# Kernel optimization log

Hardware: AMD Instinct MI355X
Metric: run time of the kernel (lower is better)

## Reference

```python
import jax, jax.numpy as jnp
import numpy as np

N, K = 262144, 8
IN_F, H_F, OUT_F = 16, 128, 16
NEG_SLOPE = 0.01  # torch LeakyReLU default


def setup_inputs() -> dict:
    key = jax.random.key(0)
    ks = jax.random.split(key, 10)
    h = jax.random.normal(ks[0], (N, IN_F), dtype=jnp.float32)
    pos = jax.random.uniform(ks[1], (N, 3), dtype=jnp.float32)
    nbr_idx = jax.random.randint(ks[2], (N, K), 0, N)

    def xavier(k, shape):
        fan_in, fan_out = shape[0], shape[1]
        a = jnp.sqrt(6.0 / (fan_in + fan_out))
        return jax.random.uniform(k, shape, jnp.float32, -a, a)

    W0 = xavier(ks[3], (K * IN_F, H_F))
    b0 = xavier(ks[4], (1, H_F))
    W1 = xavier(ks[5], (K * H_F, H_F))
    b1 = xavier(ks[6], (1, H_F))
    W2 = xavier(ks[7], (K * H_F, OUT_F))
    b2 = xavier(ks[8], (1, OUT_F))
    return {"h": h, "pos": pos, "nbr_idx": nbr_idx,
            "W0": W0, "b0": b0, "W1": W1, "b1": b1, "W2": W2, "b2": b2}


def _layer(h, pos, nbr_idx, W, b, activation):
    # gather neighbor messages and positions: [N, K, F], [N, K, 3]
    msgs = h[nbr_idx]
    src_pos = pos[nbr_idx]
    diff = pos[:, None, :] - src_pos                       # [N, K, 3]
    dist = jnp.sqrt(jnp.sum(diff * diff, axis=2, keepdims=True))  # [N, K, 1]
    dist = jnp.where(dist == 0, jnp.float32(0.5), dist)
    wow = (msgs / dist).reshape(h.shape[0], -1)            # [N, K*F]
    out = wow @ W + b
    if activation:
        out = jnp.where(out >= 0, out, NEG_SLOPE * out)
    return out


def reference(h, pos, nbr_idx, W0, b0, W1, b1, W2, b2):
    h1 = _layer(h, pos, nbr_idx, W0, b0, False)   # input layer
    h2 = _layer(h1, pos, nbr_idx, W1, b1, True)   # hidden layer (LeakyReLU)
    h3 = _layer(h2, pos, nbr_idx, W2, b2, False)  # output layer
    return h3
```

## Files before the change

### kernel.cpp

```cpp
#include <hip/hip_runtime.h>
#include <hip/hip_fp16.h>


typedef _Float16 f16x8 __attribute__((ext_vector_type(8)));
typedef float f32x4 __attribute__((ext_vector_type(4)));

#define NNODES 262144

__device__ __forceinline__ void gload_lds16(const __half* g, __half* l) {
    __builtin_amdgcn_global_load_lds(
        (const __attribute__((address_space(1))) unsigned int*)g,
        (__attribute__((address_space(3))) unsigned int*)l, 16, 0, 0);
}

__global__ __launch_bounds__(256) void conv_h_kernel(const float* __restrict__ h,
                                                     __half* __restrict__ h16, int n) {
    int i = blockIdx.x * 256 + threadIdx.x;
    if (i < n) h16[i] = __float2half(h[i]);
}

__global__ __launch_bounds__(256) void prep_edges_kernel(const float* __restrict__ pos,
                                                         const int* __restrict__ nbr,
                                                         __half* __restrict__ invd, int n_edges) {
    int e = blockIdx.x * 256 + threadIdx.x;
    if (e >= n_edges) return;
    int i = e >> 3;
    int n = nbr[e];
    float dx = pos[i * 3 + 0] - pos[n * 3 + 0];
    float dy = pos[i * 3 + 1] - pos[n * 3 + 1];
    float dz = pos[i * 3 + 2] - pos[n * 3 + 2];
    float d = sqrtf(dx * dx + dy * dy + dz * dz);
    if (d == 0.0f) d = 0.5f;
    invd[e] = __float2half((1.0f / d) * 0.00390625f);
}

__global__ __launch_bounds__(256) void shuffle_w_kernel(const float* __restrict__ W,
                                                        __half* __restrict__ Wf,
                                                        int KT, int FO) {
    int e = blockIdx.x * 256 + threadIdx.x;
    if (e >= KT * FO) return;
    int j = e & 7;
    int lane = (e >> 3) & 63;
    int rest = e >> 9;
    int NT = FO >> 4;
    int t = rest % NT;
    int s = rest / NT;
    int k = s * 32 + (lane >> 4) * 8 + j;
    int n = t * 16 + (lane & 15);
    Wf[e] = __float2half(W[k * FO + n]);
}

__global__ __launch_bounds__(256) void shuffle_w2s_kernel(const float* __restrict__ W2,
                                                          __half* __restrict__ Wf) {
    int e = blockIdx.x * 256 + threadIdx.x;
    if (e >= 128 * 128) return;
    int j = e & 7;
    int lane = (e >> 3) & 63;
    int rest = e >> 9;
    int t = rest % 8;
    int s = rest / 8;
    int k = s * 32 + (lane >> 4) * 8 + j;
    Wf[e] = __float2half(W2[(size_t)(t * 128 + k) * 16 + (lane & 15)]);
}

__global__ __launch_bounds__(256) void layer0_kernel(
    const __half* __restrict__ hprev, const __half* __restrict__ invd,
    const int* __restrict__ nbr, const __half* __restrict__ Wf,
    const float* __restrict__ bias, __half* __restrict__ outp) {
    __shared__ __align__(16) __half Bs[16384];

    const int tid = threadIdx.x;
    const int wave = tid >> 6;
    const int lane = tid & 63;
    const int quad = lane >> 4;
    const int lmod = lane & 15;
    const int mbase = blockIdx.x * 128 + wave * 16 + lmod;

    int idx[2][8];
    f16x8 invr[2];
#pragma unroll
    for (int mt = 0; mt < 2; ++mt) {
        const int m = mbase + mt * 64;
        const int4* nrow = (const int4*)(nbr + (size_t)m * 8);
        const int4 iA = nrow[0];
        const int4 iB = nrow[1];
        idx[mt][0] = iA.x; idx[mt][1] = iA.y; idx[mt][2] = iA.z; idx[mt][3] = iA.w;
        idx[mt][4] = iB.x; idx[mt][5] = iB.y; idx[mt][6] = iB.z; idx[mt][7] = iB.w;
        invr[mt] = *(const f16x8*)(invd + (size_t)m * 8);
    }

    f32x4 acc[2][8];
#pragma unroll
    for (int mt = 0; mt < 2; ++mt)
#pragma unroll
        for (int t = 0; t < 8; ++t) acc[mt][t] = f32x4{0.f, 0.f, 0.f, 0.f};

    {
        const uint4* src = (const uint4*)Wf;
        uint4* dst = (uint4*)Bs;
#pragma unroll
        for (int i = 0; i < 8; ++i) dst[i * 256 + tid] = src[i * 256 + tid];
    }
    __syncthreads();

#pragma unroll
    for (int s = 0; s < 4; ++s) {
        const int nb = 2 * s + (quad >> 1);
        f16x8 as[2];
#pragma unroll
        for (int mt = 0; mt < 2; ++mt) {
            f16x8 av = *(const f16x8*)(hprev + (size_t)idx[mt][nb] * 16 + (quad & 1) * 8);
            as[mt] = av * invr[mt][nb];
        }
#pragma unroll
        for (int t = 0; t < 8; ++t) {
            f16x8 b = *(const f16x8*)(Bs + ((size_t)(s * 8 + t) * 64 + lane) * 8);
#pragma unroll
            for (int mt = 0; mt < 2; ++mt)
                acc[mt][t] = __builtin_amdgcn_mfma_f32_16x16x32_f16(as[mt], b, acc[mt][t], 0, 0, 0);
        }
    }

#pragma unroll
    for (int mt = 0; mt < 2; ++mt) {
        const int rbase = blockIdx.x * 128 + mt * 64 + wave * 16 + quad * 4;
#pragma unroll
        for (int t = 0; t < 8; ++t) {
            const int col = t * 16 + lmod;
            const float bv = bias[col];
#pragma unroll
            for (int rr = 0; rr < 4; ++rr) {
                float v = acc[mt][t][rr] * 256.0f + bv;
                outp[(size_t)(rbase + rr) * 128 + col] = __float2half(v);
            }
        }
    }
}

__device__ __forceinline__ int off16(int seg, int row) {
    return seg * 64 + (row & ~15) + ((row ^ seg) & 15);
}

__global__ __launch_bounds__(256, 4) void layer1p_kernel(
    const __half* __restrict__ hprev, const __half* __restrict__ invd,
    const int* __restrict__ nbr, const __half* __restrict__ Wf,
    const __half* __restrict__ Wf2s, const float* __restrict__ bias,
    __half* __restrict__ Pout) {
    __shared__ __align__(16) __half As[2][8192];

    const int tid = threadIdx.x;
    const int wave = tid >> 6;
    const int lane = tid & 63;
    const int quad = lane >> 4;
    const int lmod = lane & 15;
    const int rowblk = blockIdx.x * 64;

    int grow2[4];
#pragma unroll
    for (int i = 0; i < 4; ++i) {
        const int row = (lane & 48) | ((lane & 15) ^ (wave * 4 + i));
        grow2[i] = rowblk + row;
    }

    int idxA[4], idxB[4], idxR[2][4];
#pragma unroll
    for (int i = 0; i < 4; ++i) {
        const int* nb_ = nbr + (size_t)grow2[i] * 8;
        idxA[i] = nb_[0];
        idxB[i] = nb_[1];
        idxR[0][i] = nb_[2];
    }

    f16x8 invF[4];
#pragma unroll
    for (int m = 0; m < 4; ++m)
        invF[m] = *(const f16x8*)(invd + (size_t)(rowblk + m * 16 + lmod) * 8);

    int roff4[4];
#pragma unroll
    for (int ks = 0; ks < 4; ++ks) {
        const int seg = ks * 4 + quad;
        roff4[ks] = (seg * 64 + ((lmod ^ seg) & 15)) * 8;
    }

    const __half* WfB = Wf + ((size_t)(wave * 2) * 64 + lane) * 8;

    f16x8 Bc[2][2], Bn[2][2];
#pragma unroll
    for (int ks2 = 0; ks2 < 2; ++ks2)
#pragma unroll
        for (int tl = 0; tl < 2; ++tl)
            Bc[ks2][tl] = *(const f16x8*)(WfB + (size_t)(ks2 * 8 + tl) * 512);

#pragma unroll
    for (int i = 0; i < 4; ++i)
        gload_lds16(hprev + (size_t)idxA[i] * 128 + (wave * 4 + i) * 8,
                    &As[0][(size_t)(wave * 256 + i * 64) * 8]);

    f32x4 acc[4][2];
#pragma unroll
    for (int m = 0; m < 4; ++m) { acc[m][0] = f32x4{0.f,0.f,0.f,0.f}; acc[m][1] = f32x4{0.f,0.f,0.f,0.f}; }

    __syncthreads();

#pragma unroll
    for (int nb = 0; nb < 8; ++nb) {
        const int cur = nb & 1;
        if (nb < 7) {
#pragma unroll
            for (int i = 0; i < 4; ++i) {
                const int id = (nb == 0) ? idxB[i] : idxR[(nb + 1) & 1][i];
                gload_lds16(hprev + (size_t)id * 128 + (wave * 4 + i) * 8,
                            &As[cur ^ 1][(size_t)(wave * 256 + i * 64) * 8]);
            }
        }
        if (nb < 5) {
#pragma unroll
            for (int i = 0; i < 4; ++i)
                idxR[(nb + 1) & 1][i] = nbr[(size_t)grow2[i] * 8 + nb + 3];
        }
#pragma unroll
        for (int h = 0; h < 2; ++h) {
            const int p = nb * 2 + h;
            if (p < 15) {
#pragma unroll
                for (int ks2 = 0; ks2 < 2; ++ks2)
#pragma unroll
                    for (int tl = 0; tl < 2; ++tl)
                        Bn[ks2][tl] = *(const f16x8*)(WfB + (size_t)(((p + 1) * 2 + ks2) * 8 + tl) * 512);
            }
#pragma unroll
            for (int m = 0; m < 4; ++m) {
#pragma unroll
                for (int ks2 = 0; ks2 < 2; ++ks2) {
                    const int ks = h * 2 + ks2;
                    f16x8 a = *(const f16x8*)(&As[cur][roff4[ks] + m * 128]);
                    a = a * invF[m][nb];
                    acc[m][0] = __builtin_amdgcn_mfma_f32_16x16x32_f16(a, Bc[ks2][0], acc[m][0], 0, 0, 0);
                    acc[m][1] = __builtin_amdgcn_mfma_f32_16x16x32_f16(a, Bc[ks2][1], acc[m][1], 0, 0, 0);
                }
            }
#pragma unroll
            for (int ks2 = 0; ks2 < 2; ++ks2) {
                Bc[ks2][0] = Bn[ks2][0];
                Bc[ks2][1] = Bn[ks2][1];
            }
        }
        if (nb < 7) __syncthreads();
    }

    __half* As0 = &As[0][0];
#pragma unroll
    for (int m = 0; m < 4; ++m) {
#pragma unroll
        for (int tl = 0; tl < 2; ++tl) {
            const int col = wave * 32 + tl * 16 + lmod;
            const float bv = bias[col];
            const int sg = col >> 3;
            const int jj = col & 7;
#pragma unroll
            for (int rr = 0; rr < 4; ++rr) {
                const int row = m * 16 + quad * 4 + rr;
                float v = acc[m][tl][rr] * 256.0f + bv;
                v = (v >= 0.f) ? v : 0.01f * v;
                As0[off16(sg, row) * 8 + jj] = __float2half(v);
            }
        }
    }
    __syncthreads();

    const __half* WfB2 = Wf2s + ((size_t)(wave * 2) * 64 + lane) * 8;
    f16x8 B2[4][2];
#pragma unroll
    for (int ks = 0; ks < 4; ++ks)
#pragma unroll
        for (int tl = 0; tl < 2; ++tl)
            B2[ks][tl] = *(const f16x8*)(WfB2 + (size_t)(ks * 8 + tl) * 512);

    f32x4 acc2[4][2];
#pragma unroll
    for (int m = 0; m < 4; ++m) { acc2[m][0] = f32x4{0.f,0.f,0.f,0.f}; acc2[m][1] = f32x4{0.f,0.f,0.f,0.f}; }
#pragma unroll
    for (int m = 0; m < 4; ++m) {
#pragma unroll
        for (int ks = 0; ks < 4; ++ks) {
            f16x8 a2 = *(const f16x8*)(&As0[roff4[ks] + m * 128]);
            acc2[m][0] = __builtin_amdgcn_mfma_f32_16x16x32_f16(a2, B2[ks][0], acc2[m][0], 0, 0, 0);
            acc2[m][1] = __builtin_amdgcn_mfma_f32_16x16x32_f16(a2, B2[ks][1], acc2[m][1], 0, 0, 0);
        }
    }

#pragma unroll
    for (int m = 0; m < 4; ++m) {
#pragma unroll
        for (int tl = 0; tl < 2; ++tl) {
            const int col = wave * 32 + tl * 16 + lmod;
#pragma unroll
            for (int rr = 0; rr < 4; ++rr) {
                const int grow = rowblk + m * 16 + quad * 4 + rr;
                Pout[(size_t)grow * 128 + col] = __float2half(acc2[m][tl][rr]);
            }
        }
    }
}

__global__ __launch_bounds__(256) void reduce_kernel(
    const __half* __restrict__ P, const __half* __restrict__ invd,
    const int* __restrict__ nbr, const float* __restrict__ b2,
    float* __restrict__ outp) {
    const int d = blockIdx.x * 256 + threadIdx.x;

    const int4* nrow = (const int4*)(nbr + (size_t)d * 8);
    const int4 iA = nrow[0];
    const int4 iB = nrow[1];
    const int idx[8] = {iA.x, iA.y, iA.z, iA.w, iB.x, iB.y, iB.z, iB.w};
    const f16x8 iv = *(const f16x8*)(invd + (size_t)d * 8);

    f16x8 lo[8], hi[8];
#pragma unroll
    for (int k = 0; k < 8; ++k) {
        const __half* p = P + (size_t)idx[k] * 128 + k * 16;
        lo[k] = *(const f16x8*)p;
        hi[k] = *(const f16x8*)(p + 8);
    }

    float acc[16];
#pragma unroll
    for (int c = 0; c < 16; ++c) acc[c] = 0.f;
#pragma unroll
    for (int k = 0; k < 8; ++k) {
        const float w = (float)iv[k];
#pragma unroll
        for (int c = 0; c < 8; ++c) {
            acc[c] += w * (float)lo[k][c];
            acc[c + 8] += w * (float)hi[k][c];
        }
    }

    float4 o[4];
#pragma unroll
    for (int q = 0; q < 4; ++q) {
        o[q].x = acc[q * 4 + 0] * 256.0f + b2[q * 4 + 0];
        o[q].y = acc[q * 4 + 1] * 256.0f + b2[q * 4 + 1];
        o[q].z = acc[q * 4 + 2] * 256.0f + b2[q * 4 + 2];
        o[q].w = acc[q * 4 + 3] * 256.0f + b2[q * 4 + 3];
    }
    float4* dst = (float4*)(outp + (size_t)d * 16);
#pragma unroll
    for (int q = 0; q < 4; ++q) dst[q] = o[q];
}

extern "C" void kernel_launch(void* const* d_in, const int* in_sizes, int n_in,
                              void* d_out, int out_size, void* d_ws, size_t ws_size,
                              hipStream_t stream) {
    const float* h   = (const float*)d_in[0];
    const float* pos = (const float*)d_in[1];
    const int*   nbr = (const int*)d_in[2];
    const float* W0  = (const float*)d_in[3];
    const float* b0  = (const float*)d_in[4];
    const float* W1  = (const float*)d_in[5];
    const float* b1  = (const float*)d_in[6];
    const float* W2  = (const float*)d_in[7];
    const float* b2  = (const float*)d_in[8];

    const int N = NNODES;

    char* w = (char*)d_ws;
    __half* h1 = (__half*)w;
    __half* P  = (__half*)(w + (size_t)67108864);
    __half* invd2 = (__half*)w;

    char* ob = (char*)d_out;
    __half* invd = (__half*)(ob + 0);
    __half* h16  = (__half*)(ob + 4194304);
    __half* W0f  = (__half*)(ob + 12582912);
    __half* W1f  = (__half*)(ob + 12615680);
    __half* Wf2s = (__half*)(ob + 12877824);

    conv_h_kernel<<<(N * 16 + 255) / 256, 256, 0, stream>>>(h, h16, N * 16);
    prep_edges_kernel<<<(N * 8 + 255) / 256, 256, 0, stream>>>(pos, nbr, invd, N * 8);
    shuffle_w_kernel<<<(128 * 128 + 255) / 256, 256, 0, stream>>>(W0, W0f, 128, 128);
    shuffle_w_kernel<<<(1024 * 128 + 255) / 256, 256, 0, stream>>>(W1, W1f, 1024, 128);
    shuffle_w2s_kernel<<<(128 * 128 + 255) / 256, 256, 0, stream>>>(W2, Wf2s);

    layer0_kernel<<<N / 128, 256, 0, stream>>>(h16, invd, nbr, W0f, b0, h1);
    layer1p_kernel<<<N / 64, 256, 0, stream>>>(h1, invd, nbr, W1f, Wf2s, b1, P);

    (void)hipMemcpyAsync(invd2, invd, 4194304, hipMemcpyDeviceToDevice, stream);

    reduce_kernel<<<N / 256, 256, 0, stream>>>(P, invd2, nbr, b2, (float*)d_out);
}
```

Before: 355.2 us.

## Replace direct global-to-LDS gathers with register-staged gathers pre-scaled by inverse distance

```diff
diff --git a/kernel.cpp b/kernel.cpp
--- a/kernel.cpp
+++ b/kernel.cpp
@@ -6,12 +6,6 @@
 typedef float f32x4 __attribute__((ext_vector_type(4)));
 
 #define NNODES 262144
-
-__device__ __forceinline__ void gload_lds16(const __half* g, __half* l) {
-    __builtin_amdgcn_global_load_lds(
-        (const __attribute__((address_space(1))) unsigned int*)g,
-        (__attribute__((address_space(3))) unsigned int*)l, 16, 0, 0);
-}
 
 __global__ __launch_bounds__(256) void conv_h_kernel(const float* __restrict__ h,
                                                      __half* __restrict__ h16, int n) {
@@ -154,33 +148,24 @@
     const int quad = lane >> 4;
     const int lmod = lane & 15;
     const int rowblk = blockIdx.x * 64;
-
-    int grow2[4];
+    const int seg = lmod;
+
+    const int rbase = rowblk + wave * 16 + quad;
+    const int* nbp = nbr + (size_t)rbase * 8;
+    const __half* ivp = invd + (size_t)rbase * 8;
+
+    int soff[4];
 #pragma unroll
     for (int i = 0; i < 4; ++i) {
-        const int row = (lane & 48) | ((lane & 15) ^ (wave * 4 + i));
-        grow2[i] = rowblk + row;
-    }
-
-    int idxA[4], idxB[4], idxR[2][4];
-#pragma unroll
-    for (int i = 0; i < 4; ++i) {
-        const int* nb_ = nbr + (size_t)grow2[i] * 8;
-        idxA[i] = nb_[0];
-        idxB[i] = nb_[1];
-        idxR[0][i] = nb_[2];
-    }
-
-    f16x8 invF[4];
-#pragma unroll
-    for (int m = 0; m < 4; ++m)
-        invF[m] = *(const f16x8*)(invd + (size_t)(rowblk + m * 16 + lmod) * 8);
+        const int srow = wave * 16 + i * 4 + quad;
+        soff[i] = off16(seg, srow) * 8;
+    }
 
     int roff4[4];
 #pragma unroll
     for (int ks = 0; ks < 4; ++ks) {
-        const int seg = ks * 4 + quad;
-        roff4[ks] = (seg * 64 + ((lmod ^ seg) & 15)) * 8;
+        const int sg = ks * 4 + quad;
+        roff4[ks] = (sg * 64 + ((lmod ^ sg) & 15)) * 8;
     }
 
     const __half* WfB = Wf + ((size_t)(wave * 2) * 64 + lane) * 8;
@@ -192,32 +177,50 @@
         for (int tl = 0; tl < 2; ++tl)
             Bc[ks2][tl] = *(const f16x8*)(WfB + (size_t)(ks2 * 8 + tl) * 512);
 
-#pragma unroll
-    for (int i = 0; i < 4; ++i)
-        gload_lds16(hprev + (size_t)idxA[i] * 128 + (wave * 4 + i) * 8,
-                    &As[0][(size_t)(wave * 256 + i * 64) * 8]);
+    int idxQ[2][4];
+    f16x8 ga[2][4];
+    {
+        int id0[4], id1[4];
+#pragma unroll
+        for (int i = 0; i < 4; ++i) id0[i] = nbp[i * 32 + 0];
+#pragma unroll
+        for (int i = 0; i < 4; ++i)
+            ga[0][i] = *(const f16x8*)(hprev + (size_t)id0[i] * 128 + seg * 8);
+#pragma unroll
+        for (int i = 0; i < 4; ++i) id1[i] = nbp[i * 32 + 1];
+#pragma unroll
+        for (int i = 0; i < 4; ++i)
+            ga[1][i] = *(const f16x8*)(hprev + (size_t)id1[i] * 128 + seg * 8);
+#pragma unroll
+        for (int i = 0; i < 4; ++i) idxQ[0][i] = nbp[i * 32 + 2];
+#pragma unroll
+        for (int i = 0; i < 4; ++i) idxQ[1][i] = nbp[i * 32 + 3];
+    }
+
+#pragma unroll
+    for (int i = 0; i < 4; ++i) {
+        const _Float16 sc = *(const _Float16*)(ivp + i * 32 + 0);
+        f16x8 v = ga[0][i] * sc;
+        *(f16x8*)(&As[0][soff[i]]) = v;
+    }
+    __syncthreads();
 
     f32x4 acc[4][2];
 #pragma unroll
     for (int m = 0; m < 4; ++m) { acc[m][0] = f32x4{0.f,0.f,0.f,0.f}; acc[m][1] = f32x4{0.f,0.f,0.f,0.f}; }
-
-    __syncthreads();
 
 #pragma unroll
     for (int nb = 0; nb < 8; ++nb) {
         const int cur = nb & 1;
-        if (nb < 7) {
-#pragma unroll
-            for (int i = 0; i < 4; ++i) {
-                const int id = (nb == 0) ? idxB[i] : idxR[(nb + 1) & 1][i];
-                gload_lds16(hprev + (size_t)id * 128 + (wave * 4 + i) * 8,
-                            &As[cur ^ 1][(size_t)(wave * 256 + i * 64) * 8]);
-            }
-        }
-        if (nb < 5) {
+        if (nb < 6) {
 #pragma unroll
             for (int i = 0; i < 4; ++i)
-                idxR[(nb + 1) & 1][i] = nbr[(size_t)grow2[i] * 8 + nb + 3];
+                ga[cur][i] = *(const f16x8*)(hprev + (size_t)idxQ[cur][i] * 128 + seg * 8);
+        }
+        if (nb < 4) {
+#pragma unroll
+            for (int i = 0; i < 4; ++i)
+                idxQ[cur][i] = nbp[i * 32 + nb + 4];
         }
 #pragma unroll
         for (int h = 0; h < 2; ++h) {
@@ -233,9 +236,7 @@
             for (int m = 0; m < 4; ++m) {
 #pragma unroll
                 for (int ks2 = 0; ks2 < 2; ++ks2) {
-                    const int ks = h * 2 + ks2;
-                    f16x8 a = *(const f16x8*)(&As[cur][roff4[ks] + m * 128]);
-                    a = a * invF[m][nb];
+                    f16x8 a = *(const f16x8*)(&As[cur][roff4[h * 2 + ks2] + m * 128]);
                     acc[m][0] = __builtin_amdgcn_mfma_f32_16x16x32_f16(a, Bc[ks2][0], acc[m][0], 0, 0, 0);
                     acc[m][1] = __builtin_amdgcn_mfma_f32_16x16x32_f16(a, Bc[ks2][1], acc[m][1], 0, 0, 0);
                 }
@@ -246,7 +247,15 @@
                 Bc[ks2][1] = Bn[ks2][1];
             }
         }
-        if (nb < 7) __syncthreads();
+        if (nb < 7) {
+#pragma unroll
+            for (int i = 0; i < 4; ++i) {
+                const _Float16 sc = *(const _Float16*)(ivp + i * 32 + nb + 1);
+                f16x8 v = ga[(nb + 1) & 1][i] * sc;
+                *(f16x8*)(&As[cur ^ 1][soff[i]]) = v;
+            }
+            __syncthreads();
+        }
     }
 
     __half* As0 = &As[0][0];
```

New measurement: 326.2 us. 1.09x faster.
